# Kernel optimization log

Hardware: AMD Instinct MI355X
Metric: run time of the kernel (lower is better)

The kernel has to match this reference:

```python
import jax, jax.numpy as jnp
import numpy as np

B, S, D, W, P = 32, 512, 768, 256, 1024


def setup_inputs() -> dict:
    key = jax.random.key(0)
    k_h, k_len, k_pair, k_w1, k_w2 = jax.random.split(key, 5)
    h = jax.random.normal(k_h, (B, S, D), dtype=jnp.float32)
    # ragged word spans: each word covers 1 or 2 contiguous subwords; total <= S
    word_len = jax.random.randint(k_len, (B, W), 1, 3, dtype=jnp.int32)  # in {1,2}
    word_start = jnp.concatenate(
        [jnp.zeros((B, 1), jnp.int32), jnp.cumsum(word_len, axis=1)[:, :-1]], axis=1
    )
    # word-index pairs per configuration; -1 means "use zero embedding"
    pair_idx = jax.random.randint(k_pair, (B, P, 2), 0, W + 1, dtype=jnp.int32) - 1
    w1 = jax.random.normal(k_w1, (2 * D, 300), dtype=jnp.float32) * 0.02
    b1 = jnp.zeros((300,), jnp.float32)
    w2 = jax.random.normal(k_w2, (300, 4), dtype=jnp.float32) * 0.02
    b2 = jnp.zeros((4,), jnp.float32)
    return {"h": h, "w1": w1, "b1": b1, "w2": w2, "b2": b2,
            "word_start": word_start, "word_len": word_len, "pair_idx": pair_idx}


def reference(h, w1, b1, w2, b2, word_start, word_len, pair_idx):
    # --- mean-pool subword embeddings per word via prefix sums (segment mean) ---
    csum = jnp.cumsum(h, axis=1)                                   # [B,S,D]
    csum = jnp.concatenate([jnp.zeros_like(csum[:, :1]), csum], 1)  # [B,S+1,D]
    end = word_start + word_len                                     # [B,W]
    seg_sum = (jnp.take_along_axis(csum, end[:, :, None], axis=1)
               - jnp.take_along_axis(csum, word_start[:, :, None], axis=1))
    word_emb = seg_sum / word_len[:, :, None].astype(h.dtype)       # [B,W,D]
    # --- per-pair gather with -1 -> zero vector ---
    valid = (pair_idx >= 0)                                         # [B,P,2]
    idx = jnp.maximum(pair_idx, 0).reshape(h.shape[0], -1)          # [B,2P]
    emb = jnp.take_along_axis(word_emb, idx[:, :, None], axis=1)    # [B,2P,D]
    emb = emb.reshape(pair_idx.shape[0], pair_idx.shape[1], 2, -1)
    emb = jnp.where(valid[..., None], emb, jnp.zeros((), h.dtype))
    mlp_input = emb.reshape(-1, 2 * h.shape[-1])                    # [B*P, 2D]
    # --- tiny MLP + softmax (dropout is identity in eval) ---
    x = jnp.tanh(mlp_input @ w1 + b1)
    return jax.nn.softmax(x @ w2 + b2, axis=-1)                     # [B*P, 4]
```

## Files before the change

### kernel.cpp

```cpp
#include <hip/hip_runtime.h>
#include <cstddef>
#include <cstdint>

#define Bb   32
#define Ss   512
#define Dd   768
#define Ww   256
#define Pp   1024
#define NH   300
#define SLOT1 320
#define NPAD 640
#define Mm   (Bb * Ww)

typedef __attribute__((ext_vector_type(8))) short bf16x8;
typedef __attribute__((ext_vector_type(4))) float f32x4;

#define GPTR(p) ((const __attribute__((address_space(1))) void*)(p))
#define LPTR(p) ((__attribute__((address_space(3))) void*)(p))

__device__ __forceinline__ unsigned short f2bf(float x) {
    unsigned u = __builtin_bit_cast(unsigned, x);
    u += 0x7fffu + ((u >> 16) & 1u);
    return (unsigned short)(u >> 16);
}
__device__ __forceinline__ float bf2f(unsigned short u) {
    return __builtin_bit_cast(float, (unsigned)u << 16);
}
__device__ __forceinline__ float fast_tanh(float x) {
    x = fminf(fmaxf(x, -15.0f), 15.0f);
    float e = __expf(2.0f * x);
    return 1.0f - 2.0f * __builtin_amdgcn_rcpf(e + 1.0f);
}

__global__ __launch_bounds__(256) void prep_kernel(
    const float* __restrict__ h, const float* __restrict__ w1,
    const int* __restrict__ word_start, const int* __restrict__ word_len,
    unsigned short* __restrict__ emb, unsigned short* __restrict__ bmatT,
    unsigned short* __restrict__ zrow)
{
    const int gid    = blockIdx.x * 256 + threadIdx.x;
    const int stride = 1024 * 256;

    for (int u = gid; u < Mm * 192; u += stride) {
        const int m = u / 192;
        const int c = u - m * 192;
        const int b   = m >> 8;
        const int s0  = word_start[m];
        const int len = word_len[m];
        const float* p = h + (size_t)b * (Ss * Dd) + (size_t)s0 * Dd + c * 4;
        float4 v = *(const float4*)p;
        if (len == 2) {
            float4 v2 = *(const float4*)(p + Dd);
            v.x = (v.x + v2.x) * 0.5f;
            v.y = (v.y + v2.y) * 0.5f;
            v.z = (v.z + v2.z) * 0.5f;
            v.w = (v.w + v2.w) * 0.5f;
        }
        ushort4 o = make_ushort4(f2bf(v.x), f2bf(v.y), f2bf(v.z), f2bf(v.w));
        *(ushort4*)(emb + (size_t)m * Dd + c * 4) = o;
    }

    for (int u = gid; u < Dd * NPAD; u += stride) {
        const int k = u / NPAD;
        const int n = u - k * NPAD;
        float v = 0.0f;
        if (n < NH)                            v = w1[(size_t)k * NH + n];
        else if (n >= SLOT1 && n < SLOT1 + NH) v = w1[(size_t)(Dd + k) * NH + (n - SLOT1)];
        bmatT[(size_t)n * Dd + k] = f2bf(v);
    }

    if (gid < NPAD / 4)
        *(ushort4*)(zrow + gid * 4) = make_ushort4(0, 0, 0, 0);
}

__global__ __launch_bounds__(256) void gemm_kernel(
    const unsigned short* __restrict__ emb, const unsigned short* __restrict__ bmatT,
    unsigned short* __restrict__ proj)
{
    __shared__ bf16x8 Al[2][4][128];
    __shared__ bf16x8 Bl[2][4][128];

    const int bid = blockIdx.x;
    const int t   = threadIdx.x;

    const int swz   = (bid & 7) * 40 + (bid >> 3);
    const int mBase = (swz / 5) * 128;
    const int nBase = (swz % 5) * 128;

    const int srow = t & 127;
    const int skb  = t >> 7;
    const unsigned short* srcA = emb   + (size_t)(mBase + srow) * Dd + (skb << 3);
    const unsigned short* srcB = bmatT + (size_t)(nBase + srow) * Dd + (skb << 3);
    char* ldsA = (char*)&Al[0][0][0] + t * 16;
    char* ldsB = (char*)&Bl[0][0][0] + t * 16;

    const int lane = t & 63;
    const int w    = t >> 6;
    const int wr   = w >> 1;
    const int wc   = w & 1;
    const int fr   = lane & 15;
    const int kb   = lane >> 4;

    f32x4 acc[4][4];
#pragma unroll
    for (int i = 0; i < 4; ++i)
#pragma unroll
        for (int j = 0; j < 4; ++j)
#pragma unroll
            for (int r = 0; r < 4; ++r) acc[i][j][r] = 0.0f;

#define STAGE(c, off)                                                                          \
    __builtin_amdgcn_global_load_lds(GPTR(srcA + (off)),      LPTR(ldsA + (c) * 8192),        16, 0, 0); \
    __builtin_amdgcn_global_load_lds(GPTR(srcA + (off) + 16), LPTR(ldsA + (c) * 8192 + 4096), 16, 0, 0); \
    __builtin_amdgcn_global_load_lds(GPTR(srcB + (off)),      LPTR(ldsB + (c) * 8192),        16, 0, 0); \
    __builtin_amdgcn_global_load_lds(GPTR(srcB + (off) + 16), LPTR(ldsB + (c) * 8192 + 4096), 16, 0, 0)

#define COMPUTE(c)                                                                             \
    {                                                                                          \
        bf16x8 a[4], b[4];                                                                     \
        _Pragma("unroll")                                                                      \
        for (int mi = 0; mi < 4; ++mi) a[mi] = Al[c][kb][wr * 64 + mi * 16 + fr];              \
        _Pragma("unroll")                                                                      \
        for (int ni = 0; ni < 4; ++ni) b[ni] = Bl[c][kb][wc * 64 + ni * 16 + fr];              \
        _Pragma("unroll")                                                                      \
        for (int mi = 0; mi < 4; ++mi)                                                         \
            _Pragma("unroll")                                                                  \
            for (int ni = 0; ni < 4; ++ni)                                                     \
                acc[mi][ni] = __builtin_amdgcn_mfma_f32_16x16x32_bf16(a[mi], b[ni], acc[mi][ni], 0, 0, 0); \
    }

    STAGE(0, 0);
    __syncthreads();
    int cur = 0;
    for (int k0 = 32; k0 < Dd; k0 += 32) {
        STAGE(cur ^ 1, k0);
        COMPUTE(cur);
        __syncthreads();
        cur ^= 1;
    }
    COMPUTE(cur);
#undef STAGE
#undef COMPUTE

    const int r0 = mBase + wr * 64 + kb * 4;
    const int c0 = nBase + wc * 64 + fr;
#pragma unroll
    for (int mi = 0; mi < 4; ++mi)
#pragma unroll
        for (int ni = 0; ni < 4; ++ni)
#pragma unroll
            for (int r = 0; r < 4; ++r)
                proj[(size_t)(r0 + mi * 16 + r) * NPAD + c0 + ni * 16] = f2bf(acc[mi][ni][r]);
}

__global__ __launch_bounds__(256) void mlp_kernel(
    const unsigned short* __restrict__ proj, const unsigned short* __restrict__ zrow,
    const float* __restrict__ b1, const float* __restrict__ w2,
    const float* __restrict__ b2, const int* __restrict__ pair_idx,
    float* __restrict__ out)
{
    __shared__ float red[4][64][17];

    const int wv   = threadIdx.x >> 6;
    const int wave = blockIdx.x * 4 + wv;
    const int lane = threadIdx.x & 63;
    const int wid0 = wave * 4;
    const int b    = wid0 >> 10;
    const unsigned short* base = proj + (size_t)b * (Ww * NPAD);

    const int4 piA = *(const int4*)(pair_idx + wid0 * 2);
    const int4 piB = *(const int4*)(pair_idx + wid0 * 2 + 4);
    const int idx[8] = {piA.x, piA.y, piA.z, piA.w, piB.x, piB.y, piB.z, piB.w};

    const unsigned short* r0p[4];
    const unsigned short* r1p[4];
#pragma unroll
    for (int p = 0; p < 4; ++p) {
        const int i0 = idx[p * 2], i1 = idx[p * 2 + 1];
        r0p[p] = (i0 >= 0) ? base + (size_t)i0 * NPAD : zrow;
        r1p[p] = ((i1 >= 0) ? base + (size_t)i1 * NPAD : zrow) + SLOT1;
    }

    unsigned short g0[4][5], g1[4][5];
#pragma unroll
    for (int p = 0; p < 4; ++p)
#pragma unroll
        for (int it = 0; it < 5; ++it) {
            const int j = lane + it * 64;
            g0[p][it] = r0p[p][j];
            g1[p][it] = r1p[p][j];
        }

    float acc[4][4];
#pragma unroll
    for (int p = 0; p < 4; ++p)
#pragma unroll
        for (int c = 0; c < 4; ++c) acc[p][c] = 0.0f;

#pragma unroll
    for (int it = 0; it < 5; ++it) {
        const int j  = lane + it * 64;
        const bool ok = (j < NH);
        const float bj = ok ? b1[j] : 0.0f;
        float4 wv4 = make_float4(0.f, 0.f, 0.f, 0.f);
        if (ok) wv4 = *(const float4*)(w2 + (size_t)j * 4);
#pragma unroll
        for (int p = 0; p < 4; ++p) {
            const float v = bj + bf2f(g0[p][it]) + bf2f(g1[p][it]);
            const float x = ok ? fast_tanh(v) : 0.0f;
            acc[p][0] = fmaf(x, wv4.x, acc[p][0]);
            acc[p][1] = fmaf(x, wv4.y, acc[p][1]);
            acc[p][2] = fmaf(x, wv4.z, acc[p][2]);
            acc[p][3] = fmaf(x, wv4.w, acc[p][3]);
        }
    }

#pragma unroll
    for (int p = 0; p < 4; ++p)
#pragma unroll
        for (int c = 0; c < 4; ++c)
            red[wv][lane][p * 4 + c] = acc[p][c];
    __syncthreads();

    const int o = lane >> 2;
    const int g = lane & 3;
    float v = 0.0f;
#pragma unroll
    for (int i = 0; i < 16; ++i)
        v += red[wv][g * 16 + i][o];
    v += __shfl_xor(v, 1, 64);
    v += __shfl_xor(v, 2, 64);

    const int c = o & 3;
    const float l = v + b2[c];
    float mx = fmaxf(l, __shfl_xor(l, 4, 64));
    mx = fmaxf(mx, __shfl_xor(mx, 8, 64));
    const float e = __expf(l - mx);
    float s = e + __shfl_xor(e, 4, 64);
    s += __shfl_xor(s, 8, 64);
    const float r = e * __builtin_amdgcn_rcpf(s);
    if (g == 0)
        out[(size_t)(wid0 + (o >> 2)) * 4 + c] = r;
}

extern "C" void kernel_launch(void* const* d_in, const int* in_sizes, int n_in,
                              void* d_out, int out_size, void* d_ws, size_t ws_size,
                              hipStream_t stream)
{
    const float* h          = (const float*)d_in[0];
    const float* w1         = (const float*)d_in[1];
    const float* b1         = (const float*)d_in[2];
    const float* w2         = (const float*)d_in[3];
    const float* b2         = (const float*)d_in[4];
    const int*   word_start = (const int*)d_in[5];
    const int*   word_len   = (const int*)d_in[6];
    const int*   pair_idx   = (const int*)d_in[7];
    float*       out        = (float*)d_out;

    unsigned short* proj  = (unsigned short*)d_ws;
    unsigned short* emb   = (unsigned short*)((char*)d_ws + 10485760);
    unsigned short* bmatT = (unsigned short*)((char*)d_ws + 23068672);
    unsigned short* zrow  = (unsigned short*)((char*)d_ws + 24051712);

    prep_kernel<<<dim3(1024), dim3(256), 0, stream>>>(
        h, w1, word_start, word_len, emb, bmatT, zrow);
    gemm_kernel<<<dim3(320), dim3(256), 0, stream>>>(emb, bmatT, proj);
    mlp_kernel <<<dim3(2048), dim3(256), 0, stream>>>(proj, zrow, b1, w2, b2, pair_idx, out);
}
```

Before: 52.16 us.

## Fuse subword mean-pooling into GEMM A-tile loading, drop emb buffer

Mean-pooling of subword embeddings moves from the prep kernel into the GEMM's A-operand staging: each thread loads fp32 h rows into registers, averages, converts to bf16 and writes LDS while the previous tile is computed. This removes the intermediate bf16 embedding buffer write and read-back. In exchange, h is re-read by every N-tile block, and the A path loses asynchronous global-to-LDS loads, adding register pressure and load latency inside the main loop.

```diff
diff --git a/kernel.cpp b/kernel.cpp
--- a/kernel.cpp
+++ b/kernel.cpp
@@ -26,6 +26,9 @@
 __device__ __forceinline__ float bf2f(unsigned short u) {
     return __builtin_bit_cast(float, (unsigned)u << 16);
 }
+__device__ __forceinline__ unsigned pk2(float a, float b) {
+    return (unsigned)f2bf(a) | ((unsigned)f2bf(b) << 16);
+}
 __device__ __forceinline__ float fast_tanh(float x) {
     x = fminf(fmaxf(x, -15.0f), 15.0f);
     float e = __expf(2.0f * x);
@@ -33,32 +36,11 @@
 }
 
 __global__ __launch_bounds__(256) void prep_kernel(
-    const float* __restrict__ h, const float* __restrict__ w1,
-    const int* __restrict__ word_start, const int* __restrict__ word_len,
-    unsigned short* __restrict__ emb, unsigned short* __restrict__ bmatT,
+    const float* __restrict__ w1, unsigned short* __restrict__ bmatT,
     unsigned short* __restrict__ zrow)
 {
     const int gid    = blockIdx.x * 256 + threadIdx.x;
-    const int stride = 1024 * 256;
-
-    for (int u = gid; u < Mm * 192; u += stride) {
-        const int m = u / 192;
-        const int c = u - m * 192;
-        const int b   = m >> 8;
-        const int s0  = word_start[m];
-        const int len = word_len[m];
-        const float* p = h + (size_t)b * (Ss * Dd) + (size_t)s0 * Dd + c * 4;
-        float4 v = *(const float4*)p;
-        if (len == 2) {
-            float4 v2 = *(const float4*)(p + Dd);
-            v.x = (v.x + v2.x) * 0.5f;
-            v.y = (v.y + v2.y) * 0.5f;
-            v.z = (v.z + v2.z) * 0.5f;
-            v.w = (v.w + v2.w) * 0.5f;
-        }
-        ushort4 o = make_ushort4(f2bf(v.x), f2bf(v.y), f2bf(v.z), f2bf(v.w));
-        *(ushort4*)(emb + (size_t)m * Dd + c * 4) = o;
-    }
+    const int stride = 512 * 256;
 
     for (int u = gid; u < Dd * NPAD; u += stride) {
         const int k = u / NPAD;
@@ -74,7 +56,9 @@
 }
 
 __global__ __launch_bounds__(256) void gemm_kernel(
-    const unsigned short* __restrict__ emb, const unsigned short* __restrict__ bmatT,
+    const float* __restrict__ h,
+    const int* __restrict__ word_start, const int* __restrict__ word_len,
+    const unsigned short* __restrict__ bmatT,
     unsigned short* __restrict__ proj)
 {
     __shared__ bf16x8 Al[2][4][128];
@@ -89,9 +73,15 @@
 
     const int srow = t & 127;
     const int skb  = t >> 7;
-    const unsigned short* srcA = emb   + (size_t)(mBase + srow) * Dd + (skb << 3);
-    const unsigned short* srcB = bmatT + (size_t)(nBase + srow) * Dd + (skb << 3);
-    char* ldsA = (char*)&Al[0][0][0] + t * 16;
+    const int skb8 = skb << 3;
+
+    const int arow = mBase + srow;
+    const int s0   = word_start[arow];
+    const int len  = word_len[arow];
+    const float* hp  = h + (size_t)(arow >> 8) * (Ss * Dd) + (size_t)s0 * Dd + skb8;
+    const float* hp2 = hp + (size_t)(len - 1) * Dd;
+
+    const unsigned short* srcB = bmatT + (size_t)(nBase + srow) * Dd + skb8;
     char* ldsB = (char*)&Bl[0][0][0] + t * 16;
 
     const int lane = t & 63;
@@ -109,9 +99,34 @@
 #pragma unroll
             for (int r = 0; r < 4; ++r) acc[i][j][r] = 0.0f;
 
-#define STAGE(c, off)                                                                          \
-    __builtin_amdgcn_global_load_lds(GPTR(srcA + (off)),      LPTR(ldsA + (c) * 8192),        16, 0, 0); \
-    __builtin_amdgcn_global_load_lds(GPTR(srcA + (off) + 16), LPTR(ldsA + (c) * 8192 + 4096), 16, 0, 0); \
+    float4 ax0, ax1, ax2, ax3, ay0, ay1, ay2, ay3;
+
+#define HLOAD(k0_)                                                        \
+    {                                                                     \
+        const float* p1 = hp  + (k0_);                                    \
+        const float* p2 = hp2 + (k0_);                                    \
+        ax0 = *(const float4*)(p1);      ax1 = *(const float4*)(p1 + 4);  \
+        ax2 = *(const float4*)(p1 + 16); ax3 = *(const float4*)(p1 + 20); \
+        ay0 = *(const float4*)(p2);      ay1 = *(const float4*)(p2 + 4);  \
+        ay2 = *(const float4*)(p2 + 16); ay3 = *(const float4*)(p2 + 20); \
+    }
+
+#define POOLW(c)                                                          \
+    {                                                                     \
+        union { bf16x8 v; unsigned u[4]; } oA, oB;                        \
+        oA.u[0] = pk2((ax0.x + ay0.x) * 0.5f, (ax0.y + ay0.y) * 0.5f);    \
+        oA.u[1] = pk2((ax0.z + ay0.z) * 0.5f, (ax0.w + ay0.w) * 0.5f);    \
+        oA.u[2] = pk2((ax1.x + ay1.x) * 0.5f, (ax1.y + ay1.y) * 0.5f);    \
+        oA.u[3] = pk2((ax1.z + ay1.z) * 0.5f, (ax1.w + ay1.w) * 0.5f);    \
+        oB.u[0] = pk2((ax2.x + ay2.x) * 0.5f, (ax2.y + ay2.y) * 0.5f);    \
+        oB.u[1] = pk2((ax2.z + ay2.z) * 0.5f, (ax2.w + ay2.w) * 0.5f);    \
+        oB.u[2] = pk2((ax3.x + ay3.x) * 0.5f, (ax3.y + ay3.y) * 0.5f);    \
+        oB.u[3] = pk2((ax3.z + ay3.z) * 0.5f, (ax3.w + ay3.w) * 0.5f);    \
+        Al[c][skb][srow]     = oA.v;                                      \
+        Al[c][skb + 2][srow] = oB.v;                                      \
+    }
+
+#define STAGEB(c, off)                                                                         \
     __builtin_amdgcn_global_load_lds(GPTR(srcB + (off)),      LPTR(ldsB + (c) * 8192),        16, 0, 0); \
     __builtin_amdgcn_global_load_lds(GPTR(srcB + (off) + 16), LPTR(ldsB + (c) * 8192 + 4096), 16, 0, 0)
 
@@ -129,17 +144,24 @@
                 acc[mi][ni] = __builtin_amdgcn_mfma_f32_16x16x32_bf16(a[mi], b[ni], acc[mi][ni], 0, 0, 0); \
     }
 
-    STAGE(0, 0);
+    HLOAD(0);
+    STAGEB(0, 0);
+    POOLW(0);
     __syncthreads();
+
     int cur = 0;
     for (int k0 = 32; k0 < Dd; k0 += 32) {
-        STAGE(cur ^ 1, k0);
+        HLOAD(k0);
+        STAGEB(cur ^ 1, k0);
         COMPUTE(cur);
+        POOLW(cur ^ 1);
         __syncthreads();
         cur ^= 1;
     }
     COMPUTE(cur);
-#undef STAGE
+#undef HLOAD
+#undef POOLW
+#undef STAGEB
 #undef COMPUTE
 
     const int r0 = mBase + wr * 64 + kb * 4;
@@ -258,12 +280,10 @@
     float*       out        = (float*)d_out;
 
     unsigned short* proj  = (unsigned short*)d_ws;
-    unsigned short* emb   = (unsigned short*)((char*)d_ws + 10485760);
-    unsigned short* bmatT = (unsigned short*)((char*)d_ws + 23068672);
-    unsigned short* zrow  = (unsigned short*)((char*)d_ws + 24051712);
-
-    prep_kernel<<<dim3(1024), dim3(256), 0, stream>>>(
-        h, w1, word_start, word_len, emb, bmatT, zrow);
-    gemm_kernel<<<dim3(320), dim3(256), 0, stream>>>(emb, bmatT, proj);
+    unsigned short* bmatT = (unsigned short*)((char*)d_ws + 10485760);
+    unsigned short* zrow  = (unsigned short*)((char*)d_ws + 11468800);
+
+    prep_kernel<<<dim3(512),  dim3(256), 0, stream>>>(w1, bmatT, zrow);
+    gemm_kernel<<<dim3(320),  dim3(256), 0, stream>>>(h, word_start, word_len, bmatT, proj);
     mlp_kernel <<<dim3(2048), dim3(256), 0, stream>>>(proj, zrow, b1, w2, b2, pair_idx, out);
 }
```

Result: slower. 82.40 us (+58.0%).

## Split GEMM K dimension in two and triple-buffer LDS with explicit waitcnt

Applied to the files above, without the earlier changes.

The projection GEMM now splits K=768 into two halves, so it launches 640 blocks instead of 320 to fill more CUs, and writes two partial bf16 projection buffers. The MLP kernel gathers from both buffers and sums the partials, and each buffer carries its own zero row. The GEMM main loop moves to a three-stage LDS ring with manual vmcnt waits and barriers so global loads overlap compute more deeply. The cost is twice the proj write and gather traffic, plus an extra bf16 rounding on each partial sum.

```diff
diff --git a/kernel.cpp b/kernel.cpp
--- a/kernel.cpp
+++ b/kernel.cpp
@@ -11,6 +11,11 @@
 #define SLOT1 320
 #define NPAD 640
 #define Mm   (Bb * Ww)
+#define ZROW 8192
+#define ZOFF (ZROW * NPAD)
+#define PBUF ((Mm + 1) * NPAD)
+#define KH   384
+#define NST  12
 
 typedef __attribute__((ext_vector_type(8))) short bf16x8;
 typedef __attribute__((ext_vector_type(4))) float f32x4;
@@ -36,7 +41,7 @@
     const float* __restrict__ h, const float* __restrict__ w1,
     const int* __restrict__ word_start, const int* __restrict__ word_len,
     unsigned short* __restrict__ emb, unsigned short* __restrict__ bmatT,
-    unsigned short* __restrict__ zrow)
+    unsigned short* __restrict__ proj)
 {
     const int gid    = blockIdx.x * 256 + threadIdx.x;
     const int stride = 1024 * 256;
@@ -69,28 +74,33 @@
         bmatT[(size_t)n * Dd + k] = f2bf(v);
     }
 
-    if (gid < NPAD / 4)
-        *(ushort4*)(zrow + gid * 4) = make_ushort4(0, 0, 0, 0);
+    if (gid < NPAD / 4) {
+        *(ushort4*)(proj + ZOFF + gid * 4)        = make_ushort4(0, 0, 0, 0);
+        *(ushort4*)(proj + PBUF + ZOFF + gid * 4) = make_ushort4(0, 0, 0, 0);
+    }
 }
 
 __global__ __launch_bounds__(256) void gemm_kernel(
     const unsigned short* __restrict__ emb, const unsigned short* __restrict__ bmatT,
     unsigned short* __restrict__ proj)
 {
-    __shared__ bf16x8 Al[2][4][128];
-    __shared__ bf16x8 Bl[2][4][128];
+    __shared__ bf16x8 Al[3][4][128];
+    __shared__ bf16x8 Bl[3][4][128];
 
     const int bid = blockIdx.x;
     const int t   = threadIdx.x;
 
-    const int swz   = (bid & 7) * 40 + (bid >> 3);
-    const int mBase = (swz / 5) * 128;
-    const int nBase = (swz % 5) * 128;
+    const int swz   = (bid & 7) * 80 + (bid >> 3);
+    const int kh    = swz / 320;
+    const int tIdx  = swz - kh * 320;
+    const int mBase = (tIdx / 5) * 128;
+    const int nBase = (tIdx % 5) * 128;
+    const int kOff  = kh * KH;
 
     const int srow = t & 127;
-    const int skb  = t >> 7;
-    const unsigned short* srcA = emb   + (size_t)(mBase + srow) * Dd + (skb << 3);
-    const unsigned short* srcB = bmatT + (size_t)(nBase + srow) * Dd + (skb << 3);
+    const int skb8 = (t >> 7) << 3;
+    const unsigned short* srcA = emb   + (size_t)(mBase + srow) * Dd + kOff + skb8;
+    const unsigned short* srcB = bmatT + (size_t)(nBase + srow) * Dd + kOff + skb8;
     char* ldsA = (char*)&Al[0][0][0] + t * 16;
     char* ldsB = (char*)&Bl[0][0][0] + t * 16;
 
@@ -129,19 +139,27 @@
                 acc[mi][ni] = __builtin_amdgcn_mfma_f32_16x16x32_bf16(a[mi], b[ni], acc[mi][ni], 0, 0, 0); \
     }
 
+#define KSTEP(k, cnt)                                                     \
+    asm volatile("s_waitcnt vmcnt(" #cnt ")" ::: "memory");               \
+    __builtin_amdgcn_sched_barrier(0);                                    \
+    __builtin_amdgcn_s_barrier();                                         \
+    asm volatile("" ::: "memory");                                        \
+    __builtin_amdgcn_sched_barrier(0);                                    \
+    COMPUTE((k) % 3);                                                     \
+    if ((k) < NST - 2) { STAGE((k + 2) % 3, (k + 2) * 32); }
+
     STAGE(0, 0);
-    __syncthreads();
-    int cur = 0;
-    for (int k0 = 32; k0 < Dd; k0 += 32) {
-        STAGE(cur ^ 1, k0);
-        COMPUTE(cur);
-        __syncthreads();
-        cur ^= 1;
-    }
-    COMPUTE(cur);
+    STAGE(1, 32);
+
+    KSTEP(0, 4)  KSTEP(1, 4)  KSTEP(2, 4)  KSTEP(3, 4)
+    KSTEP(4, 4)  KSTEP(5, 4)  KSTEP(6, 4)  KSTEP(7, 4)
+    KSTEP(8, 4)  KSTEP(9, 4)  KSTEP(10, 4) KSTEP(11, 0)
+
+#undef KSTEP
 #undef STAGE
 #undef COMPUTE
 
+    unsigned short* projh = proj + (size_t)kh * PBUF;
     const int r0 = mBase + wr * 64 + kb * 4;
     const int c0 = nBase + wc * 64 + fr;
 #pragma unroll
@@ -150,11 +168,11 @@
         for (int ni = 0; ni < 4; ++ni)
 #pragma unroll
             for (int r = 0; r < 4; ++r)
-                proj[(size_t)(r0 + mi * 16 + r) * NPAD + c0 + ni * 16] = f2bf(acc[mi][ni][r]);
+                projh[(size_t)(r0 + mi * 16 + r) * NPAD + c0 + ni * 16] = f2bf(acc[mi][ni][r]);
 }
 
 __global__ __launch_bounds__(256) void mlp_kernel(
-    const unsigned short* __restrict__ proj, const unsigned short* __restrict__ zrow,
+    const unsigned short* __restrict__ proj,
     const float* __restrict__ b1, const float* __restrict__ w2,
     const float* __restrict__ b2, const int* __restrict__ pair_idx,
     float* __restrict__ out)
@@ -166,29 +184,31 @@
     const int lane = threadIdx.x & 63;
     const int wid0 = wave * 4;
     const int b    = wid0 >> 10;
-    const unsigned short* base = proj + (size_t)b * (Ww * NPAD);
+    const int rbase = b * Ww * NPAD;
+    const unsigned short* proj1 = proj + PBUF;
 
     const int4 piA = *(const int4*)(pair_idx + wid0 * 2);
     const int4 piB = *(const int4*)(pair_idx + wid0 * 2 + 4);
     const int idx[8] = {piA.x, piA.y, piA.z, piA.w, piB.x, piB.y, piB.z, piB.w};
 
-    const unsigned short* r0p[4];
-    const unsigned short* r1p[4];
+    int off0[4], off1[4];
 #pragma unroll
     for (int p = 0; p < 4; ++p) {
         const int i0 = idx[p * 2], i1 = idx[p * 2 + 1];
-        r0p[p] = (i0 >= 0) ? base + (size_t)i0 * NPAD : zrow;
-        r1p[p] = ((i1 >= 0) ? base + (size_t)i1 * NPAD : zrow) + SLOT1;
-    }
-
-    unsigned short g0[4][5], g1[4][5];
+        off0[p] = (i0 >= 0) ? rbase + i0 * NPAD : ZOFF;
+        off1[p] = ((i1 >= 0) ? rbase + i1 * NPAD : ZOFF) + SLOT1;
+    }
+
+    unsigned short g0a[4][5], g0b[4][5], g1a[4][5], g1b[4][5];
 #pragma unroll
     for (int p = 0; p < 4; ++p)
 #pragma unroll
         for (int it = 0; it < 5; ++it) {
             const int j = lane + it * 64;
-            g0[p][it] = r0p[p][j];
-            g1[p][it] = r1p[p][j];
+            g0a[p][it] = proj [(size_t)off0[p] + j];
+            g0b[p][it] = proj1[(size_t)off0[p] + j];
+            g1a[p][it] = proj [(size_t)off1[p] + j];
+            g1b[p][it] = proj1[(size_t)off1[p] + j];
         }
 
     float acc[4][4];
@@ -206,7 +226,8 @@
         if (ok) wv4 = *(const float4*)(w2 + (size_t)j * 4);
 #pragma unroll
         for (int p = 0; p < 4; ++p) {
-            const float v = bj + bf2f(g0[p][it]) + bf2f(g1[p][it]);
+            const float v = bj + (bf2f(g0a[p][it]) + bf2f(g0b[p][it]))
+                               + (bf2f(g1a[p][it]) + bf2f(g1b[p][it]));
             const float x = ok ? fast_tanh(v) : 0.0f;
             acc[p][0] = fmaf(x, wv4.x, acc[p][0]);
             acc[p][1] = fmaf(x, wv4.y, acc[p][1]);
@@ -258,12 +279,11 @@
     float*       out        = (float*)d_out;
 
     unsigned short* proj  = (unsigned short*)d_ws;
-    unsigned short* emb   = (unsigned short*)((char*)d_ws + 10485760);
-    unsigned short* bmatT = (unsigned short*)((char*)d_ws + 23068672);
-    unsigned short* zrow  = (unsigned short*)((char*)d_ws + 24051712);
+    unsigned short* emb   = (unsigned short*)((char*)d_ws + 20975616);
+    unsigned short* bmatT = (unsigned short*)((char*)d_ws + 33558528);
 
     prep_kernel<<<dim3(1024), dim3(256), 0, stream>>>(
-        h, w1, word_start, word_len, emb, bmatT, zrow);
-    gemm_kernel<<<dim3(320), dim3(256), 0, stream>>>(emb, bmatT, proj);
-    mlp_kernel <<<dim3(2048), dim3(256), 0, stream>>>(proj, zrow, b1, w2, b2, pair_idx, out);
-}
+        h, w1, word_start, word_len, emb, bmatT, proj);
+    gemm_kernel<<<dim3(640),  dim3(256), 0, stream>>>(emb, bmatT, proj);
+    mlp_kernel <<<dim3(2048), dim3(256), 0, stream>>>(proj, b1, w2, b2, pair_idx, out);
+}
```

Result: slower. 55.63 us (+6.7%).
